# Kernel tuning notes

Measured on AMD Instinct MI355X. Metric: run time of the kernel, lower is better.

The kernel has to match this reference:

```python
import jax, jax.numpy as jnp
import numpy as np

# Dimensions: S tokens, H hidden, fused QKV out = DQ + 2*DKV (MHA: DQ == DKV),
# N adapters, LoRA rank R (A buffer holds 3*R: rank-chunks for q, k, v).
S, H, R, N = 4096, 4096, 16, 8
DQ, DKV = 4096, 4096


def setup_inputs() -> dict:
    key = jax.random.key(0)
    ks = jax.random.split(key, 6)
    x = jax.random.normal(ks[0], (S, H), dtype=jnp.float32)
    W_base = jax.random.normal(ks[1], (H, DQ + 2 * DKV), dtype=jnp.float32) * 0.02
    A_qkv = jax.random.normal(ks[2], (N, H, 3 * R), dtype=jnp.float32) * 0.02
    B_q = jax.random.normal(ks[3], (N, R, DQ), dtype=jnp.float32) * 0.02
    B_kv = jax.random.normal(ks[4], (N, R, 2 * DKV), dtype=jnp.float32) * 0.02
    weight_indices = jax.random.randint(ks[5], (S,), 0, N, dtype=jnp.int32)
    return {"x": x, "weight_indices": weight_indices, "W_base": W_base,
            "A_qkv": A_qkv, "B_q": B_q, "B_kv": B_kv}


def reference(x, weight_indices, W_base, A_qkv, B_q, B_kv):
    # Base fused QKV projection: [S, DQ + 2*DKV]
    base = x @ W_base
    rank = A_qkv.shape[2] // 3
    b_dim_q = B_q.shape[2]
    b_dim_kv = B_kv.shape[2] // 2
    n_adapters = A_qkv.shape[0]

    # Per-token indexed LoRA (ldmm): for token t with adapter a = indices[t],
    #   delta[t] = (x[t] @ A[a, :, chunk]) @ B[a].
    # Delta-weight (quantized) buffers are empty (set_topping_info with None),
    # so ldmm reduces to the LoRA term. We loop over the small fixed set of
    # adapters, masking tokens, instead of gathering [S,H,3R] per-token weights.
    delta = jnp.zeros_like(base)
    for a in range(n_adapters):
        m = (weight_indices == a).astype(x.dtype)[:, None]  # [S,1]
        xa = (m * x) @ A_qkv[a]                              # [S, 3R]
        oq = xa[:, 0:rank] @ B_q[a]                          # [S, DQ]
        ok = xa[:, rank:2 * rank] @ B_kv[a][:, :b_dim_kv]    # [S, DKV]
        ov = xa[:, 2 * rank:3 * rank] @ B_kv[a][:, b_dim_kv:]
        delta = delta.at[:, 0:b_dim_q].add(oq)
        delta = delta.at[:, b_dim_kv:2 * b_dim_kv].add(ok)
        delta = delta.at[:, 2 * b_dim_kv:3 * b_dim_kv].add(ov)
    return base + delta
```

## Files before the change

kernel.cpp:

```cpp
#include <hip/hip_runtime.h>

#define S_TOK 4096
#define H_DIM 4096
#define NOUT  12288
#define KBIG  4480
#define NADP  8
#define RANK  16
#define NT    (KBIG / 64)

typedef __bf16 bf16x8 __attribute__((ext_vector_type(8)));
typedef float  f32x4  __attribute__((ext_vector_type(4)));

__device__ __forceinline__ unsigned short f2bf(float f) {
  union { float f; unsigned int u; } v; v.f = f;
  unsigned int u = v.u;
  unsigned int r = (u + 0x7FFFu + ((u >> 16) & 1u)) >> 16;
  return (unsigned short)r;
}

__device__ __forceinline__ void gload_lds16(const void* g, void* l) {
  __builtin_amdgcn_global_load_lds(
      (const __attribute__((address_space(1))) void*)g,
      (__attribute__((address_space(3))) void*)l,
      16, 0, 0);
}

__global__ __launch_bounds__(256) void transpose_convert_w(
    const float* __restrict__ W, unsigned short* __restrict__ WbigT) {
  __shared__ float tile[64][65];
  const int n0 = blockIdx.x * 64;
  const int k0 = blockIdx.y * 64;
  const int tid = threadIdx.x;
  const int c = tid & 63;
  const int rb = tid >> 6;
#pragma unroll
  for (int p = 0; p < 16; ++p) {
    int r = p * 4 + rb;
    tile[r][c] = W[(size_t)(k0 + r) * NOUT + n0 + c];
  }
  __syncthreads();
#pragma unroll
  for (int p = 0; p < 16; ++p) {
    int nr = p * 4 + rb;
    WbigT[(size_t)(n0 + nr) * KBIG + k0 + c] = f2bf(tile[c][nr]);
  }
}

__global__ __launch_bounds__(384) void build_bfull(
    const float* __restrict__ Bq, const float* __restrict__ Bkv,
    unsigned short* __restrict__ WbigT) {
  const int n = blockIdx.x;
  const int tid = threadIdx.x;
  const int a = tid / 48;
  const int c = tid % 48;
  float v = 0.0f;
  if (c < 16) {
    if (n < 4096) v = Bq[(size_t)(a * RANK + c) * 4096 + n];
  } else if (c < 32) {
    if (n >= 4096 && n < 8192) v = Bkv[(size_t)(a * RANK + (c - 16)) * 8192 + (n - 4096)];
  } else {
    if (n >= 8192) v = Bkv[(size_t)(a * RANK + (c - 32)) * 8192 + (n - 4096)];
  }
  WbigT[(size_t)n * KBIG + H_DIM + tid] = f2bf(v);
}

__global__ __launch_bounds__(256) void convert_a(
    const float* __restrict__ A, unsigned short* __restrict__ Abf) {
  const int i = blockIdx.x * 256 + threadIdx.x;
  const float4 v = ((const float4*)A)[i];
  ushort4 o;
  o.x = f2bf(v.x); o.y = f2bf(v.y); o.z = f2bf(v.z); o.w = f2bf(v.w);
  ((ushort4*)Abf)[i] = o;
}

__global__ __launch_bounds__(256) void lora_a_fused(
    const float* __restrict__ x, const int* __restrict__ widx,
    const unsigned short* __restrict__ Abf, unsigned short* __restrict__ xbig) {
  const int t = blockIdx.x;
  const int tid = threadIdx.x;
  const int a = widx[t];
  float acc[48];
#pragma unroll
  for (int j = 0; j < 48; ++j) acc[j] = 0.0f;
  const float* xr = x + (size_t)t * H_DIM;
  unsigned short* o = xbig + (size_t)t * KBIG;
#pragma unroll 1
  for (int hb = 0; hb < 16; ++hb) {
    const int h = hb * 256 + tid;
    const float xv = xr[h];
    o[h] = f2bf(xv);
    const uint4* Ar = (const uint4*)(Abf + ((size_t)a * H_DIM + h) * 48);
#pragma unroll
    for (int q = 0; q < 6; ++q) {
      uint4 av = Ar[q];
      unsigned int uu[4] = {av.x, av.y, av.z, av.w};
#pragma unroll
      for (int e = 0; e < 4; ++e) {
        float lo = __uint_as_float(uu[e] << 16);
        float hi = __uint_as_float(uu[e] & 0xffff0000u);
        acc[q * 8 + 2 * e]     += xv * lo;
        acc[q * 8 + 2 * e + 1] += xv * hi;
      }
    }
  }
  if (tid < 384) {
    int j = tid - a * 48;
    if (j < 0 || j >= 48) o[H_DIM + tid] = 0;
  }
#pragma unroll
  for (int j = 0; j < 48; ++j) {
    float v = acc[j];
#pragma unroll
    for (int m = 32; m >= 1; m >>= 1) v += __shfl_xor(v, m, 64);
    acc[j] = v;
  }
  __shared__ float red[4][48];
  if ((tid & 63) == 0) {
    const int w = tid >> 6;
#pragma unroll
    for (int j = 0; j < 48; ++j) red[w][j] = acc[j];
  }
  __syncthreads();
  if (tid < 48) {
    float s = red[0][tid] + red[1][tid] + red[2][tid] + red[3][tid];
    o[H_DIM + a * 48 + tid] = f2bf(s);
  }
}

__global__ __launch_bounds__(512, 2) void gemm_bf16_8ph(
    const unsigned short* __restrict__ Xb, const unsigned short* __restrict__ Wt,
    float* __restrict__ out) {
  __shared__ __align__(16) unsigned char lds[2 * 2 * 2 * 16384];

  const int tid = threadIdx.x;
  const int w   = tid >> 6;
  const int l   = tid & 63;
  const int wm  = w >> 2;
  const int wn  = w & 3;
  const int lr  = l & 15;
  const int hi  = l >> 4;
  const int innsw = (lr & 7) << 4;

  const int id  = blockIdx.x;
  const int swz = (id & 7) * 96 + (id >> 3);
  const int bm = swz / 48, bn = swz % 48;
  const int m0 = bm * 256, n0 = bn * 256;

  auto stage = [&](int buf, int ab, int half, const unsigned short* G,
                   int row0, int kb) {
    unsigned char* lb = &lds[((((buf << 1) | ab) << 1) | half) * 16384];
    const char* gb = (const char*)G;
#pragma unroll
    for (int ld = 0; ld < 2; ++ld) {
      int d = (ld * 512 + tid) * 16;
      int row = d >> 7;
      int colb = (d & 127) ^ ((row & 7) << 4);
      gload_lds16(gb + (size_t)(row0 + row) * (KBIG * 2) + kb * 2 + colb,
                  lb + d);
    }
  };
  auto readA = [&](int buf, int mq, int mf, int kk) -> bf16x8 {
    const unsigned char* lb = &lds[((((buf << 1) | 0) << 1) | mq) * 16384];
    int ph = (wm * 64 + mf * 16 + lr) * 128 + ((kk * 64 + hi * 16) ^ innsw);
    return *(const bf16x8*)(lb + ph);
  };
  auto readB = [&](int buf, int nq, int nf, int kk) -> bf16x8 {
    const unsigned char* lb = &lds[((((buf << 1) | 1) << 1) | nq) * 16384];
    int ph = (wn * 32 + nf * 16 + lr) * 128 + ((kk * 64 + hi * 16) ^ innsw);
    return *(const bf16x8*)(lb + ph);
  };

  f32x4 acc[4][4][2];
  const f32x4 fzero = {0.f, 0.f, 0.f, 0.f};
#pragma unroll
  for (int q = 0; q < 4; ++q)
#pragma unroll
    for (int mf = 0; mf < 4; ++mf)
#pragma unroll
      for (int nf = 0; nf < 2; ++nf) acc[q][mf][nf] = fzero;

  bf16x8 a_[4][2];
  bf16x8 b0_[2][2];
  bf16x8 b1_[2][2];

#define MFMA_QUAD(Q, BSRC)                                                   \
    _Pragma("unroll") for (int kk = 0; kk < 2; ++kk)                         \
      _Pragma("unroll") for (int mf = 0; mf < 4; ++mf)                       \
        _Pragma("unroll") for (int nf = 0; nf < 2; ++nf)                     \
          acc[Q][mf][nf] = __builtin_amdgcn_mfma_f32_16x16x32_bf16(          \
              a_[mf][kk], BSRC[nf][kk], acc[Q][mf][nf], 0, 0, 0)

  stage(0, 0, 0, Xb, m0,       0);
  stage(0, 1, 0, Wt, n0,       0);
  stage(0, 1, 1, Wt, n0 + 128, 0);
  stage(0, 0, 1, Xb, m0 + 128, 0);
  asm volatile("s_waitcnt vmcnt(4)" ::: "memory");
  __builtin_amdgcn_s_barrier();

  for (int t = 0; t < NT; ++t) {
    const int cur = t & 1, nxt = cur ^ 1;
    const int tn = (t + 1 < NT) ? (t + 1) : t;
    const int kb_next = tn * 64;

#pragma unroll
    for (int mf = 0; mf < 4; ++mf)
#pragma unroll
      for (int kk = 0; kk < 2; ++kk) a_[mf][kk] = readA(cur, 0, mf, kk);
#pragma unroll
    for (int nf = 0; nf < 2; ++nf)
#pragma unroll
      for (int kk = 0; kk < 2; ++kk) b0_[nf][kk] = readB(cur, 0, nf, kk);
    stage(nxt, 0, 0, Xb, m0, kb_next);
    __builtin_amdgcn_s_barrier();
    __builtin_amdgcn_s_setprio(1);
    MFMA_QUAD(0, b0_);
    __builtin_amdgcn_s_setprio(0);
    asm volatile("s_waitcnt vmcnt(4)" ::: "memory");
    __builtin_amdgcn_s_barrier();

#pragma unroll
    for (int nf = 0; nf < 2; ++nf)
#pragma unroll
      for (int kk = 0; kk < 2; ++kk) b1_[nf][kk] = readB(cur, 1, nf, kk);
    stage(nxt, 1, 0, Wt, n0, kb_next);
    __builtin_amdgcn_s_barrier();
    __builtin_amdgcn_s_setprio(1);
    MFMA_QUAD(1, b1_);
    __builtin_amdgcn_s_setprio(0);
    asm volatile("s_waitcnt vmcnt(4)" ::: "memory");
    __builtin_amdgcn_s_barrier();

#pragma unroll
    for (int mf = 0; mf < 4; ++mf)
#pragma unroll
      for (int kk = 0; kk < 2; ++kk) a_[mf][kk] = readA(cur, 1, mf, kk);
    stage(nxt, 1, 1, Wt, n0 + 128, kb_next);
    __builtin_amdgcn_s_barrier();
    __builtin_amdgcn_s_setprio(1);
    MFMA_QUAD(2, b1_);
    __builtin_amdgcn_s_setprio(0);
    __builtin_amdgcn_s_barrier();

    stage(nxt, 0, 1, Xb, m0 + 128, kb_next);
    __builtin_amdgcn_s_barrier();
    __builtin_amdgcn_s_setprio(1);
    MFMA_QUAD(3, b0_);
    __builtin_amdgcn_s_setprio(0);
    asm volatile("s_waitcnt vmcnt(4)" ::: "memory");
    __builtin_amdgcn_s_barrier();
  }
#undef MFMA_QUAD

  const int r4 = hi * 4;
  constexpr int QM[4] = {0, 0, 1, 1};
  constexpr int QN[4] = {0, 1, 1, 0};
#pragma unroll
  for (int q = 0; q < 4; ++q)
#pragma unroll
    for (int mf = 0; mf < 4; ++mf)
#pragma unroll
      for (int nf = 0; nf < 2; ++nf) {
        const int row = m0 + QM[q] * 128 + wm * 64 + mf * 16 + r4;
        const int col = n0 + QN[q] * 128 + wn * 32 + nf * 16 + lr;
#pragma unroll
        for (int r = 0; r < 4; ++r)
          out[(size_t)(row + r) * NOUT + col] = acc[q][mf][nf][r];
      }
}

extern "C" void kernel_launch(void* const* d_in, const int* in_sizes, int n_in,
                              void* d_out, int out_size, void* d_ws, size_t ws_size,
                              hipStream_t stream) {
  const float* x    = (const float*)d_in[0];
  const int*   widx = (const int*)d_in[1];
  const float* W    = (const float*)d_in[2];
  const float* Aq   = (const float*)d_in[3];
  const float* Bq   = (const float*)d_in[4];
  const float* Bkv  = (const float*)d_in[5];
  float* out = (float*)d_out;

  unsigned short* xbig  = (unsigned short*)d_ws;
  unsigned short* WbigT = (unsigned short*)((char*)d_ws + (size_t)S_TOK * KBIG * 2);
  unsigned short* Abf   = (unsigned short*)((char*)d_ws + (size_t)S_TOK * KBIG * 2
                                            + (size_t)NOUT * KBIG * 2);

  hipLaunchKernelGGL(transpose_convert_w, dim3(NOUT / 64, H_DIM / 64), dim3(256), 0, stream, W, WbigT);
  hipLaunchKernelGGL(build_bfull, dim3(NOUT), dim3(384), 0, stream, Bq, Bkv, WbigT);
  hipLaunchKernelGGL(convert_a, dim3(NADP * H_DIM * 48 / (256 * 4)), dim3(256), 0, stream, Aq, Abf);
  hipLaunchKernelGGL(lora_a_fused, dim3(S_TOK), dim3(256), 0, stream, x, widx, Abf, xbig);
  hipLaunchKernelGGL(gemm_bf16_8ph, dim3(768), dim3(512), 0, stream, xbig, WbigT, out);
}
```

Before: 564.6 us.

## Compute LoRA-A projection with an MFMA GEMM over all adapters and reschedule staging

Replaces the per-token scalar LoRA-A kernel with a separate bf16 conversion of x, a transpose of A, and an MFMA GEMM that computes x against all 8 adapters' A (384 columns), then masks to the token's adapter while writing into the augmented input. This does 8x redundant FLOPs but moves them onto matrix cores instead of scalar FMAs with irregular gathers. The main GEMM loop also issues its four stage loads earlier, two per phase, with adjusted vmcnt waits and one fewer barrier, to deepen prefetch overlap.

```diff
diff --git a/kernel.cpp b/kernel.cpp
--- a/kernel.cpp
+++ b/kernel.cpp
@@ -64,67 +64,115 @@
   WbigT[(size_t)n * KBIG + H_DIM + tid] = f2bf(v);
 }
 
-__global__ __launch_bounds__(256) void convert_a(
-    const float* __restrict__ A, unsigned short* __restrict__ Abf) {
-  const int i = blockIdx.x * 256 + threadIdx.x;
-  const float4 v = ((const float4*)A)[i];
-  ushort4 o;
-  o.x = f2bf(v.x); o.y = f2bf(v.y); o.z = f2bf(v.z); o.w = f2bf(v.w);
-  ((ushort4*)Abf)[i] = o;
-}
-
-__global__ __launch_bounds__(256) void lora_a_fused(
-    const float* __restrict__ x, const int* __restrict__ widx,
-    const unsigned short* __restrict__ Abf, unsigned short* __restrict__ xbig) {
+__global__ __launch_bounds__(256) void convert_x(
+    const float* __restrict__ x, unsigned short* __restrict__ xbig) {
   const int t = blockIdx.x;
   const int tid = threadIdx.x;
-  const int a = widx[t];
-  float acc[48];
-#pragma unroll
-  for (int j = 0; j < 48; ++j) acc[j] = 0.0f;
-  const float* xr = x + (size_t)t * H_DIM;
-  unsigned short* o = xbig + (size_t)t * KBIG;
-#pragma unroll 1
-  for (int hb = 0; hb < 16; ++hb) {
-    const int h = hb * 256 + tid;
-    const float xv = xr[h];
-    o[h] = f2bf(xv);
-    const uint4* Ar = (const uint4*)(Abf + ((size_t)a * H_DIM + h) * 48);
-#pragma unroll
-    for (int q = 0; q < 6; ++q) {
-      uint4 av = Ar[q];
-      unsigned int uu[4] = {av.x, av.y, av.z, av.w};
-#pragma unroll
-      for (int e = 0; e < 4; ++e) {
-        float lo = __uint_as_float(uu[e] << 16);
-        float hi = __uint_as_float(uu[e] & 0xffff0000u);
-        acc[q * 8 + 2 * e]     += xv * lo;
-        acc[q * 8 + 2 * e + 1] += xv * hi;
+  const float4* xr = (const float4*)(x + (size_t)t * H_DIM);
+  ushort4* o = (ushort4*)(xbig + (size_t)t * KBIG);
+#pragma unroll
+  for (int p = 0; p < 4; ++p) {
+    float4 v = xr[p * 256 + tid];
+    ushort4 u;
+    u.x = f2bf(v.x); u.y = f2bf(v.y); u.z = f2bf(v.z); u.w = f2bf(v.w);
+    o[p * 256 + tid] = u;
+  }
+}
+
+__global__ __launch_bounds__(256) void transpose_convert_a(
+    const float* __restrict__ A, unsigned short* __restrict__ AT) {
+  __shared__ float t[128][49];
+  const int a = blockIdx.x;
+  const int h0 = blockIdx.y * 128;
+  const int tid = threadIdx.x;
+  const float* src = A + ((size_t)a * H_DIM + h0) * 48;
+#pragma unroll
+  for (int e = 0; e < 24; ++e) {
+    int idx = e * 256 + tid;
+    t[idx / 48][idx % 48] = src[idx];
+  }
+  __syncthreads();
+#pragma unroll
+  for (int e = 0; e < 24; ++e) {
+    int idx = e * 256 + tid;
+    int j = idx >> 7;
+    int c = idx & 127;
+    AT[(size_t)(a * 48 + j) * H_DIM + h0 + c] = f2bf(t[c][j]);
+  }
+}
+
+__global__ __launch_bounds__(256) void xa_gemm_scatter(
+    const unsigned short* __restrict__ Xb, const unsigned short* __restrict__ AT,
+    const int* __restrict__ widx, unsigned short* __restrict__ xbig) {
+  __shared__ __align__(16) unsigned char lds[2 * 16384];
+  const int tid = threadIdx.x;
+  const int w = tid >> 6, l = tid & 63;
+  const int wm = w >> 1, wn = w & 1;
+  const int lr = l & 15, hi = l >> 4;
+  const int innsw = (lr & 7) << 4;
+  const int m0 = blockIdx.y * 128;
+  const int n0 = blockIdx.x * 128;
+
+  f32x4 acc[4][4];
+  const f32x4 fzero = {0.f, 0.f, 0.f, 0.f};
+#pragma unroll
+  for (int mf = 0; mf < 4; ++mf)
+#pragma unroll
+    for (int nf = 0; nf < 4; ++nf) acc[mf][nf] = fzero;
+
+  for (int kt = 0; kt < H_DIM / 64; ++kt) {
+    __syncthreads();
+    const int kb = kt * 64;
+#pragma unroll
+    for (int ld = 0; ld < 4; ++ld) {
+      int d = (ld * 256 + tid) * 16;
+      int row = d >> 7;
+      int colb = (d & 127) ^ ((row & 7) << 4);
+      gload_lds16((const char*)Xb + (size_t)(m0 + row) * (KBIG * 2) + kb * 2 + colb,
+                  &lds[d]);
+    }
+#pragma unroll
+    for (int ld = 0; ld < 4; ++ld) {
+      int d = (ld * 256 + tid) * 16;
+      int row = d >> 7;
+      int colb = (d & 127) ^ ((row & 7) << 4);
+      gload_lds16((const char*)AT + (size_t)(n0 + row) * (H_DIM * 2) + kb * 2 + colb,
+                  &lds[16384 + d]);
+    }
+    __syncthreads();
+#pragma unroll
+    for (int kk = 0; kk < 2; ++kk) {
+      bf16x8 af[4], bfr[4];
+#pragma unroll
+      for (int mf = 0; mf < 4; ++mf)
+        af[mf] = *(const bf16x8*)(lds + (wm * 64 + mf * 16 + lr) * 128 +
+                                  ((kk * 64 + hi * 16) ^ innsw));
+#pragma unroll
+      for (int nf = 0; nf < 4; ++nf)
+        bfr[nf] = *(const bf16x8*)(lds + 16384 + (wn * 64 + nf * 16 + lr) * 128 +
+                                   ((kk * 64 + hi * 16) ^ innsw));
+#pragma unroll
+      for (int mf = 0; mf < 4; ++mf)
+#pragma unroll
+        for (int nf = 0; nf < 4; ++nf)
+          acc[mf][nf] = __builtin_amdgcn_mfma_f32_16x16x32_bf16(
+              af[mf], bfr[nf], acc[mf][nf], 0, 0, 0);
+    }
+  }
+  const int r4 = hi * 4;
+#pragma unroll
+  for (int mf = 0; mf < 4; ++mf)
+#pragma unroll
+    for (int r = 0; r < 4; ++r) {
+      const int t = m0 + wm * 64 + mf * 16 + r4 + r;
+      const int a = widx[t];
+#pragma unroll
+      for (int nf = 0; nf < 4; ++nf) {
+        const int col = n0 + wn * 64 + nf * 16 + lr;
+        float v = (col / 48 == a) ? acc[mf][nf][r] : 0.0f;
+        xbig[(size_t)t * KBIG + H_DIM + col] = f2bf(v);
       }
     }
-  }
-  if (tid < 384) {
-    int j = tid - a * 48;
-    if (j < 0 || j >= 48) o[H_DIM + tid] = 0;
-  }
-#pragma unroll
-  for (int j = 0; j < 48; ++j) {
-    float v = acc[j];
-#pragma unroll
-    for (int m = 32; m >= 1; m >>= 1) v += __shfl_xor(v, m, 64);
-    acc[j] = v;
-  }
-  __shared__ float red[4][48];
-  if ((tid & 63) == 0) {
-    const int w = tid >> 6;
-#pragma unroll
-    for (int j = 0; j < 48; ++j) red[w][j] = acc[j];
-  }
-  __syncthreads();
-  if (tid < 48) {
-    float s = red[0][tid] + red[1][tid] + red[2][tid] + red[3][tid];
-    o[H_DIM + a * 48 + tid] = f2bf(s);
-  }
 }
 
 __global__ __launch_bounds__(512, 2) void gemm_bf16_8ph(
@@ -211,38 +259,37 @@
 #pragma unroll
       for (int kk = 0; kk < 2; ++kk) b0_[nf][kk] = readB(cur, 0, nf, kk);
     stage(nxt, 0, 0, Xb, m0, kb_next);
+    stage(nxt, 1, 0, Wt, n0, kb_next);
     __builtin_amdgcn_s_barrier();
     __builtin_amdgcn_s_setprio(1);
     MFMA_QUAD(0, b0_);
     __builtin_amdgcn_s_setprio(0);
-    asm volatile("s_waitcnt vmcnt(4)" ::: "memory");
+    asm volatile("s_waitcnt vmcnt(6)" ::: "memory");
     __builtin_amdgcn_s_barrier();
 
 #pragma unroll
     for (int nf = 0; nf < 2; ++nf)
 #pragma unroll
       for (int kk = 0; kk < 2; ++kk) b1_[nf][kk] = readB(cur, 1, nf, kk);
-    stage(nxt, 1, 0, Wt, n0, kb_next);
+    stage(nxt, 1, 1, Wt, n0 + 128, kb_next);
+    stage(nxt, 0, 1, Xb, m0 + 128, kb_next);
     __builtin_amdgcn_s_barrier();
     __builtin_amdgcn_s_setprio(1);
     MFMA_QUAD(1, b1_);
     __builtin_amdgcn_s_setprio(0);
-    asm volatile("s_waitcnt vmcnt(4)" ::: "memory");
+    asm volatile("s_waitcnt vmcnt(8)" ::: "memory");
     __builtin_amdgcn_s_barrier();
 
 #pragma unroll
     for (int mf = 0; mf < 4; ++mf)
 #pragma unroll
       for (int kk = 0; kk < 2; ++kk) a_[mf][kk] = readA(cur, 1, mf, kk);
-    stage(nxt, 1, 1, Wt, n0 + 128, kb_next);
     __builtin_amdgcn_s_barrier();
     __builtin_amdgcn_s_setprio(1);
     MFMA_QUAD(2, b1_);
     __builtin_amdgcn_s_setprio(0);
     __builtin_amdgcn_s_barrier();
 
-    stage(nxt, 0, 1, Xb, m0 + 128, kb_next);
-    __builtin_amdgcn_s_barrier();
     __builtin_amdgcn_s_setprio(1);
     MFMA_QUAD(3, b0_);
     __builtin_amdgcn_s_setprio(0);
@@ -281,12 +328,13 @@
 
   unsigned short* xbig  = (unsigned short*)d_ws;
   unsigned short* WbigT = (unsigned short*)((char*)d_ws + (size_t)S_TOK * KBIG * 2);
-  unsigned short* Abf   = (unsigned short*)((char*)d_ws + (size_t)S_TOK * KBIG * 2
+  unsigned short* AT    = (unsigned short*)((char*)d_ws + (size_t)S_TOK * KBIG * 2
                                             + (size_t)NOUT * KBIG * 2);
 
   hipLaunchKernelGGL(transpose_convert_w, dim3(NOUT / 64, H_DIM / 64), dim3(256), 0, stream, W, WbigT);
   hipLaunchKernelGGL(build_bfull, dim3(NOUT), dim3(384), 0, stream, Bq, Bkv, WbigT);
-  hipLaunchKernelGGL(convert_a, dim3(NADP * H_DIM * 48 / (256 * 4)), dim3(256), 0, stream, Aq, Abf);
-  hipLaunchKernelGGL(lora_a_fused, dim3(S_TOK), dim3(256), 0, stream, x, widx, Abf, xbig);
+  hipLaunchKernelGGL(convert_x, dim3(S_TOK), dim3(256), 0, stream, x, xbig);
+  hipLaunchKernelGGL(transpose_convert_a, dim3(NADP, H_DIM / 128), dim3(256), 0, stream, Aq, AT);
+  hipLaunchKernelGGL(xa_gemm_scatter, dim3(3, S_TOK / 128), dim3(256), 0, stream, xbig, AT, widx, xbig);
   hipLaunchKernelGGL(gemm_bf16_8ph, dim3(768), dim3(512), 0, stream, xbig, WbigT, out);
 }
```

Result: faster. 542.4 us (-3.9%).
